# Performance work log

Hardware: AMD Instinct MI355X
Metric: run time of the kernel (lower is better)

Reference implementation:

```python
import jax, jax.numpy as jnp
import numpy as np

N = 65536      # collocation points
HID = 256      # hidden_dim
D = 3          # input_dim (x, y, t)
O = 2          # output_dim (streamfunction s, pressure p)


def _xavier(k, shape):
    fan_out, fan_in = shape
    std = (2.0 / (fan_in + fan_out)) ** 0.5
    return std * jax.random.normal(k, shape, dtype=jnp.float32)


def setup_inputs() -> dict:
    key = jax.random.key(0)
    ks = jax.random.split(key, 16)
    z = lambda n: jnp.zeros((n,), dtype=jnp.float32)
    return {
        "x": jax.random.normal(ks[0], (N,), dtype=jnp.float32),
        "y": jax.random.normal(ks[1], (N,), dtype=jnp.float32),
        "t": jax.random.normal(ks[2], (N,), dtype=jnp.float32),
        "p": jax.random.normal(ks[3], (N,), dtype=jnp.float32),
        "u": jax.random.normal(ks[4], (N,), dtype=jnp.float32),
        "v": jax.random.normal(ks[5], (N,), dtype=jnp.float32),
        # shared trunk: 3 Linear+Tanh layers
        "W1": _xavier(ks[6], (HID, D)),   "b1": z(HID),
        "W2": _xavier(ks[7], (HID, HID)), "b2": z(HID),
        "W3": _xavier(ks[8], (HID, HID)), "b3": z(HID),
        # pde head
        "Wp1": _xavier(ks[9], (HID, HID)),  "bp1": z(HID),
        "Wp2": _xavier(ks[10], (O, HID)),   "bp2": z(O),
        # data head
        "Wd1": _xavier(ks[11], (HID, HID)), "bd1": z(HID),
        "Wd2": _xavier(ks[12], (O, HID)),   "bd2": z(O),
        "lam1": jnp.float32(1.0),
        "lam2": jnp.float32(0.2),
    }


def reference(x, y, t, p, u, v,
              W1, b1, W2, b2, W3, b3,
              Wp1, bp1, Wp2, bp2,
              Wd1, bd1, Wd2, bd2,
              lam1, lam2):
    def trunk(q):  # q: [3]
        h = jnp.tanh(W1 @ q + b1)
        h = jnp.tanh(W2 @ h + b2)
        h = jnp.tanh(W3 @ h + b3)
        return h

    def pde_out(q):
        return Wp2 @ jnp.tanh(Wp1 @ trunk(q) + bp1) + bp2  # [2]

    def data_out(q):
        return Wd2 @ jnp.tanh(Wd1 @ trunk(q) + bd1) + bd2  # [2]

    s_pde = lambda q: pde_out(q)[0]
    p_pde = lambda q: pde_out(q)[1]
    s_data = lambda q: data_out(q)[0]

    grad_s = jax.grad(s_pde)                 # [3]  (s_x, s_y, s_t)
    hess_s = jax.jacfwd(grad_s)              # [3,3]
    third_s = jax.jacfwd(hess_s)             # [3,3,3]

    def per_sample(q):
        g1 = grad_s(q)
        H2 = hess_s(q)
        T3 = third_s(q)
        gp = jax.grad(p_pde)(q)
        do = data_out(q)
        gsd = jax.grad(s_data)(q)

        u_ = g1[1]            # u = ds/dy
        v_ = -g1[0]           # v = -ds/dx
        u_x, u_y, u_t = H2[1, 0], H2[1, 1], H2[1, 2]
        v_x, v_y, v_t = -H2[0, 0], -H2[0, 1], -H2[0, 2]
        u_xx, u_yy = T3[1, 0, 0], T3[1, 1, 1]
        v_xx, v_yy = -T3[0, 0, 0], -T3[0, 1, 1]
        p_x, p_y = gp[0], gp[1]

        f_ = lam1 * (u_t + u_ * u_x + v_ * u_y) + p_x - lam2 * (u_xx + u_yy)
        g_ = lam1 * (v_t + u_ * v_x + v_ * v_y) + p_y - lam2 * (v_xx + v_yy)

        p_pred = do[1]        # data head pressure
        u_pred = gsd[1]       # d s_data / dy
        v_pred = -gsd[0]      # -d s_data / dx
        return p_pred, u_pred, v_pred, f_, g_

    q = jnp.stack([x, y, t], axis=1)  # [N, 3]
    p_pred, u_pred, v_pred, f_, g_ = jax.vmap(per_sample)(q)
    return p_pred, u_pred, v_pred, f_, g_
```

## Files before the change

### kernel.cpp

```cpp
#include <hip/hip_runtime.h>


#define N_PTS 65536
#define HID   256
#define TS    6
#define MROWS (TS * 13)
#define MT    5

typedef _Float16 half_t;
typedef __attribute__((ext_vector_type(8))) _Float16 half8;
typedef __attribute__((ext_vector_type(4))) float floatx4;

#define J_HI   0
#define REDBUF 39936
#define LDS_BYTES (REDBUF + 288)

struct alignas(4) hpair { half_t a, b; };

__device__ __forceinline__ float fast_tanh(float x) {
    float e = __builtin_amdgcn_exp2f(x * 2.885390081777927f);
    return 1.f - 2.f * __builtin_amdgcn_rcpf(e + 1.f);
}

__device__ __forceinline__ void tanh_jet(const float* u, float* h) {
    const float f  = fast_tanh(u[0]);
    const float f1 = 1.f - f * f;
    const float f2 = -2.f * f * f1;
    const float f3 = -2.f * f1 * f1 + 4.f * f * f * f1;
    const float ux = u[1], uy = u[2], ut = u[3];
    const float uxx = u[4], uxy = u[5], uyy = u[6], uxt = u[7], uyt = u[8];
    h[0] = f;
    h[1] = f1 * ux;  h[2] = f1 * uy;  h[3] = f1 * ut;
    h[4] = f2 * ux * ux + f1 * uxx;
    h[5] = f2 * ux * uy + f1 * uxy;
    h[6] = f2 * uy * uy + f1 * uyy;
    h[7] = f2 * ux * ut + f1 * uxt;
    h[8] = f2 * uy * ut + f1 * uyt;
    h[9]  = f3 * ux * ux * ux + 3.f * f2 * ux * uxx + f1 * u[9];
    h[10] = f3 * ux * ux * uy + f2 * (uxx * uy + 2.f * uxy * ux) + f1 * u[10];
    h[11] = f3 * ux * uy * uy + f2 * (uyy * ux + 2.f * uxy * uy) + f1 * u[11];
    h[12] = f3 * uy * uy * uy + 3.f * f2 * uy * uyy + f1 * u[12];
}

__global__ void prep_w(const float* __restrict__ W2, const float* __restrict__ W3,
                       const float* __restrict__ Wp1, const float* __restrict__ Wd1,
                       half_t* __restrict__ ws) {
    int idx = blockIdx.x * 256 + threadIdx.x;
#pragma unroll
    for (int r = 0; r < 4; ++r) {
        int e = idx + r * 65536;
        int m = e >> 16, i = e & 65535;
        const float* src = (m == 0) ? W2 : (m == 1) ? W3 : (m == 2) ? Wp1 : Wd1;
        float w = src[i];
        half_t hi = (half_t)w;
        half_t lo = (half_t)(w - (float)hi);
        int n = i >> 8, k = i & 255;
        int addr = (((n >> 4) * 8 + (k >> 5)) * 64 + ((k >> 3) & 3) * 16 + (n & 15)) * 8
                   + (k & 7);
        ws[m * 131072 + addr] = hi;
        ws[m * 131072 + 65536 + addr] = lo;
    }
}

__device__ __forceinline__ void load_B(const half_t* bh, int vo, int kb,
                                       half8 (&Bh)[4]) {
#pragma unroll
    for (int nt = 0; nt < 4; ++nt) {
        int off = nt * 4096 + kb * 512 + vo;
        Bh[nt] = *(const half8*)(bh + off);
    }
}

__device__ __forceinline__ void mfma_phase(const char* __restrict__ smem,
                                           const int (&mx)[MT], const int (&mr)[MT],
                                           int kb, int q,
                                           const half8 (&Bh)[4],
                                           floatx4 (&acc)[MT][4]) {
    const int kq = (kb * 4 + q) << 4;
    __builtin_amdgcn_s_setprio(1);
#pragma unroll
    for (int mt = 0; mt < MT; ++mt) {
        const int a = mr[mt] + (kq ^ mx[mt]);
        half8 Ah = *(const half8*)(smem + J_HI + a);
#pragma unroll
        for (int nt = 0; nt < 4; ++nt) {
            acc[mt][nt] = __builtin_amdgcn_mfma_f32_16x16x32_f16(Ah, Bh[nt], acc[mt][nt], 0, 0, 0);
        }
    }
    __builtin_amdgcn_s_setprio(0);
}

__device__ __forceinline__ void epilogue_roll(char* __restrict__ smem,
                                              const float* __restrict__ bias,
                                              int wave, int lane,
                                              floatx4 (&acc)[MT][4]) {
    const int n = wave * 64 + lane;
    const float bn = bias[n];
    const int lanebase = ((n >> 3) << 4) | ((n & 7) << 1);
    float cprev[16], ccur[16];
    const int s_lo[MT] = {0, 1, 2, 3, 4};
    const int s_hi[MT] = {0, 1, 2, 3, 5};
#pragma unroll
    for (int mt = 0; mt < MT; ++mt) {
        float tv[4][4];
#pragma unroll
        for (int j = 0; j < 4; ++j)
#pragma unroll
            for (int r = 0; r < 4; ++r) tv[j][r] = acc[mt][j][r];
#pragma unroll
        for (int r = 0; r < 4; ++r) {
            asm("v_permlane16_swap_b32 %0, %1" : "+v"(tv[0][r]), "+v"(tv[1][r]));
            asm("v_permlane16_swap_b32 %0, %1" : "+v"(tv[2][r]), "+v"(tv[3][r]));
            asm("v_permlane32_swap_b32 %0, %1" : "+v"(tv[0][r]), "+v"(tv[2][r]));
            asm("v_permlane32_swap_b32 %0, %1" : "+v"(tv[1][r]), "+v"(tv[3][r]));
        }
#pragma unroll
        for (int j = 0; j < 4; ++j)
#pragma unroll
            for (int r = 0; r < 4; ++r) ccur[j * 4 + r] = tv[j][r];
#pragma unroll
        for (int s = s_lo[mt]; s <= s_hi[mt]; ++s) {
            float u[13], h[13];
#pragma unroll
            for (int c = 0; c < 13; ++c) {
                const int row = 13 * s + c;
                u[c] = ((row >> 4) == mt) ? ccur[row & 15] : cprev[row & 15];
            }
            u[0] += bn;
            tanh_jet(u, h);
#pragma unroll
            for (int c = 0; c < 13; ++c) {
                const int m = 13 * s + c;
                const int off = m * 512 + (lanebase ^ ((m & 15) << 4));
                *(half_t*)(smem + J_HI + off) = (half_t)h[c];
            }
        }
#pragma unroll
        for (int i = 0; i < 16; ++i) cprev[i] = ccur[i];
    }
}

__device__ __forceinline__ void layer(char* __restrict__ smem,
                                      const half_t* bh,
                                      const float* __restrict__ bias,
                                      int wave, int lane, int vo, int q, int nl,
                                      const half_t* nbh,
                                      half8 (&P0h)[4],
                                      floatx4 (&acc)[MT][4]) {
    int mx[MT], mr[MT];
#pragma unroll
    for (int mt = 0; mt < MT; ++mt) {
        int m = mt * 16 + nl;
        if (m > MROWS - 1) m = MROWS - 1;
        mx[mt] = (m & 15) << 4;
        mr[mt] = m * 512;
    }
    half8 B1h[4], B2h[4];
    load_B(bh, vo, 1, B1h);
#pragma unroll
    for (int mt = 0; mt < MT; ++mt)
#pragma unroll
        for (int nt = 0; nt < 4; ++nt) acc[mt][nt] = floatx4{0.f, 0.f, 0.f, 0.f};
    mfma_phase(smem, mx, mr, 0, q, P0h, acc);
    load_B(bh, vo, 2, B2h);
    mfma_phase(smem, mx, mr, 1, q, B1h, acc);
#pragma unroll 1
    for (int kb = 2; kb < 8; kb += 2) {
        load_B(bh, vo, kb + 1, B1h);
        mfma_phase(smem, mx, mr, kb, q, B2h, acc);
        if (kb + 2 < 8) load_B(bh, vo, kb + 2, B2h);
        mfma_phase(smem, mx, mr, kb + 1, q, B1h, acc);
    }
    load_B(nbh, vo, 0, P0h);
    __syncthreads();
    epilogue_roll(smem, bias, wave, lane, acc);
    __syncthreads();
}

__device__ __forceinline__ void head_phase(const char* __restrict__ smem,
                                           const int (&mh)[2], int kb, int q,
                                           const half8 (&Bh)[4],
                                           floatx4 (&hacc)[2][4]) {
    __builtin_amdgcn_s_setprio(1);
#pragma unroll
    for (int ht = 0; ht < 2; ++ht) {
        const int a = mh[ht] * 512 + ((((kb * 4 + q) << 4)) ^ ((mh[ht] & 15) << 4));
        half8 Ah = *(const half8*)(smem + J_HI + a);
#pragma unroll
        for (int nt = 0; nt < 4; ++nt) {
            hacc[ht][nt] = __builtin_amdgcn_mfma_f32_16x16x32_f16(Ah, Bh[nt], hacc[ht][nt], 0, 0, 0);
        }
    }
    __builtin_amdgcn_s_setprio(0);
}

__global__ __launch_bounds__(256, 3) void pinn_mfma(
    const float* __restrict__ gx, const float* __restrict__ gy, const float* __restrict__ gt,
    const float* __restrict__ W1, const float* __restrict__ b1,
    const float* __restrict__ b2, const float* __restrict__ b3,
    const float* __restrict__ bp1, const float* __restrict__ Wp2,
    const float* __restrict__ bd1, const float* __restrict__ Wd2,
    const float* __restrict__ bd2,
    const float* __restrict__ lam1p, const float* __restrict__ lam2p,
    const half_t* __restrict__ wsw, float* __restrict__ out) {
    extern __shared__ char smem[];
    const int t = threadIdx.x;
    const int wave = t >> 6, lane = t & 63;
    const int q = lane >> 4, nl = lane & 15;
    const int base = blockIdx.x * TS;
    const int wo = __builtin_amdgcn_readfirstlane(wave) * 16384;
    const int vo = lane * 8;

    const half_t* W2h = wsw + wo;
    const half_t* W3h = wsw + 131072 + wo;
    const half_t* Wph = wsw + 2 * 131072 + wo;
    const half_t* Wdh = wsw + 3 * 131072 + wo;

    half8 P0h[4];
    load_B(W2h, vo, 0, P0h);

#pragma unroll 1
    for (int ii = 0; ii < 3; ++ii) {
        int p = ii * 256 + t;
        int s = p >> 7, j = (p & 127) * 2;
        int gi = base + s; if (gi >= N_PTS) gi = N_PTS - 1;
        float qx = gx[gi], qy = gy[gi], qt = gt[gi];
        float hv[2][13];
#pragma unroll
        for (int d = 0; d < 2; ++d) {
            int jj = j + d;
            float w0 = W1[3 * jj], w1 = W1[3 * jj + 1], w2 = W1[3 * jj + 2];
            float f = fast_tanh(w0 * qx + w1 * qy + w2 * qt + b1[jj]);
            float f1 = 1.f - f * f;
            float f2c = -2.f * f * f1;
            float f3c = -2.f * f1 * f1 + 4.f * f * f * f1;
            float* h = hv[d];
            h[0] = f; h[1] = f1 * w0; h[2] = f1 * w1; h[3] = f1 * w2;
            h[4] = f2c * w0 * w0; h[5] = f2c * w0 * w1; h[6] = f2c * w1 * w1;
            h[7] = f2c * w0 * w2; h[8] = f2c * w1 * w2;
            h[9]  = f3c * w0 * w0 * w0; h[10] = f3c * w0 * w0 * w1;
            h[11] = f3c * w0 * w1 * w1; h[12] = f3c * w1 * w1 * w1;
        }
#pragma unroll
        for (int c = 0; c < 13; ++c) {
            int m = s * 13 + c;
            int off = m * 512 + ((((j) >> 3) ^ (m & 15)) << 4) + ((j & 7) << 1);
            half_t hA = (half_t)hv[0][c], hB = (half_t)hv[1][c];
            *(hpair*)(smem + J_HI + off) = hpair{hA, hB};
        }
    }
    __syncthreads();

    floatx4 acc[MT][4];

    layer(smem, W2h, b2, wave, lane, vo, q, nl, W3h, P0h, acc);
    layer(smem, W3h, b3, wave, lane, vo, q, nl, Wdh, P0h, acc);

    {
        int ch = (nl & 3) == 3 ? 0 : (nl & 3);
        int mh[2];
        mh[0] = (nl >> 2) * 13 + ch;
        {
            int s1 = 4 + (nl >> 2);
            mh[1] = (s1 < TS) ? s1 * 13 + ch : 52;
        }
        floatx4 hacc[2][4];
#pragma unroll
        for (int ht = 0; ht < 2; ++ht)
#pragma unroll
            for (int nt = 0; nt < 4; ++nt) hacc[ht][nt] = floatx4{0.f, 0.f, 0.f, 0.f};
        head_phase(smem, mh, 0, q, P0h, hacc);
#pragma unroll 1
        for (int kb = 1; kb < 8; ++kb) {
            half8 Bh[4];
            load_B(Wdh, vo, kb, Bh);
            head_phase(smem, mh, kb, q, Bh, hacc);
        }
        load_B(Wph, vo, 0, P0h);
        float* rb = (float*)(smem + REDBUF);
#pragma unroll
        for (int ht = 0; ht < 2; ++ht) {
            float pp = 0, up = 0, vp = 0;
#pragma unroll
            for (int nt = 0; nt < 4; ++nt) {
                int n = wave * 64 + nt * 16 + nl;
                floatx4 a = hacc[ht][nt];
                float f = fast_tanh(a.x + bd1[n]);
                float f1 = 1.f - f * f;
                float hdx = f1 * a.y, hdy = f1 * a.z;
                float w0 = Wd2[n], w1 = Wd2[HID + n];
                pp += w1 * f;
                up += w0 * hdy;
                vp -= w0 * hdx;
            }
#pragma unroll
            for (int msk = 1; msk < 16; msk <<= 1) {
                pp += __shfl_xor(pp, msk, 64);
                up += __shfl_xor(up, msk, 64);
                vp += __shfl_xor(vp, msk, 64);
            }
            int s = ht * 4 + q;
            if (nl == 0 && s < TS) {
                rb[(s * 4 + wave) * 3 + 0] = pp;
                rb[(s * 4 + wave) * 3 + 1] = up;
                rb[(s * 4 + wave) * 3 + 2] = vp;
            }
        }
        __syncthreads();
        if (t < TS && base + t < N_PTS) {
            float P = 0, U = 0, V = 0;
#pragma unroll
            for (int w = 0; w < 4; ++w) {
                P += rb[(t * 4 + w) * 3 + 0];
                U += rb[(t * 4 + w) * 3 + 1];
                V += rb[(t * 4 + w) * 3 + 2];
            }
            out[0 * N_PTS + base + t] = P + bd2[1];
            out[1 * N_PTS + base + t] = U;
            out[2 * N_PTS + base + t] = V;
        }
    }

    layer(smem, Wph, bp1, wave, lane, vo, q, nl, Wdh, P0h, acc);

    {
        int s = t >> 5, gl = t & 31;
        if (s < TS) {
            floatx4 w0a = *(const floatx4*)(Wp2 + gl * 8);
            floatx4 w0b = *(const floatx4*)(Wp2 + gl * 8 + 4);
            floatx4 w1a = *(const floatx4*)(Wp2 + HID + gl * 8);
            floatx4 w1b = *(const floatx4*)(Wp2 + HID + gl * 8 + 4);
            float wr0[8] = {w0a.x, w0a.y, w0a.z, w0a.w, w0b.x, w0b.y, w0b.z, w0b.w};
            float wr1[8] = {w1a.x, w1a.y, w1a.z, w1a.w, w1b.x, w1b.y, w1b.z, w1b.w};
            float S[13], px = 0.f, py = 0.f;
#pragma unroll
            for (int c = 0; c < 13; ++c) {
                const int m = s * 13 + c;
                const int off = m * 512 + ((gl ^ (m & 15)) << 4);
                half8 hv = *(const half8*)(smem + J_HI + off);
                float p = 0.f, p2 = 0.f;
#pragma unroll
                for (int e = 0; e < 8; ++e) {
                    float val = (float)hv[e];
                    p += val * wr0[e];
                    if (c == 1 || c == 2) p2 += val * wr1[e];
                }
#pragma unroll
                for (int msk = 1; msk < 32; msk <<= 1) p += __shfl_xor(p, msk, 64);
                S[c] = p;
                if (c == 1) {
#pragma unroll
                    for (int msk = 1; msk < 32; msk <<= 1) p2 += __shfl_xor(p2, msk, 64);
                    px = p2;
                } else if (c == 2) {
#pragma unroll
                    for (int msk = 1; msk < 32; msk <<= 1) p2 += __shfl_xor(p2, msk, 64);
                    py = p2;
                }
            }
            if (gl == 0 && base + s < N_PTS) {
                const float lam1 = lam1p[0], lam2 = lam2p[0];
                const float u_ = S[2], v_ = -S[1];
                const float u_x = S[5], u_y = S[6], u_t = S[8];
                const float v_x = -S[4], v_y = -S[5], v_t = -S[7];
                const float u_xx = S[10], u_yy = S[12];
                const float v_xx = -S[9], v_yy = -S[11];
                const float f_ = lam1 * (u_t + u_ * u_x + v_ * u_y) + px - lam2 * (u_xx + u_yy);
                const float g_ = lam1 * (v_t + u_ * v_x + v_ * v_y) + py - lam2 * (v_xx + v_yy);
                out[3 * N_PTS + base + s] = f_;
                out[4 * N_PTS + base + s] = g_;
            }
        }
    }
}

extern "C" void kernel_launch(void* const* d_in, const int* in_sizes, int n_in,
                              void* d_out, int out_size, void* d_ws, size_t ws_size,
                              hipStream_t stream) {
    const float* x   = (const float*)d_in[0];
    const float* y   = (const float*)d_in[1];
    const float* tt  = (const float*)d_in[2];
    const float* W1  = (const float*)d_in[6];
    const float* b1  = (const float*)d_in[7];
    const float* W2  = (const float*)d_in[8];
    const float* b2  = (const float*)d_in[9];
    const float* W3  = (const float*)d_in[10];
    const float* b3  = (const float*)d_in[11];
    const float* Wp1 = (const float*)d_in[12];
    const float* bp1 = (const float*)d_in[13];
    const float* Wp2 = (const float*)d_in[14];
    const float* Wd1 = (const float*)d_in[16];
    const float* bd1 = (const float*)d_in[17];
    const float* Wd2 = (const float*)d_in[18];
    const float* bd2 = (const float*)d_in[19];
    const float* l1  = (const float*)d_in[20];
    const float* l2  = (const float*)d_in[21];
    float* out = (float*)d_out;
    half_t* wsw = (half_t*)d_ws;

    prep_w<<<256, 256, 0, stream>>>(W2, W3, Wp1, Wd1, wsw);

    (void)hipFuncSetAttribute((const void*)pinn_mfma,
                              hipFuncAttributeMaxDynamicSharedMemorySize,
                              (int)LDS_BYTES);
    pinn_mfma<<<(N_PTS + TS - 1) / TS, 256, LDS_BYTES, stream>>>(
        x, y, tt, W1, b1, b2, b3, bp1, Wp2, bd1, Wd2, bd2, l1, l2, wsw, out);
}
```

Baseline: 571.4 us.

## Shrink per-block tile from 6 to 4 samples to remove padded MFMA rows

Each block now handles 4 collocation points instead of 6. That gives 52 jet rows across 4 MFMA M-tiles (64 rows) instead of 78 rows across 5 tiles (80 rows). The head pass needs only one M-tile, and the bounds checks are gone because 65536 divides evenly by 4. The aim is less wasted MFMA work per sample and less LDS per block. In exchange, the per-layer weight loads are shared by fewer samples, so weight traffic per point rises, and there are more blocks to launch.

```diff
diff --git a/kernel.cpp b/kernel.cpp
--- a/kernel.cpp
+++ b/kernel.cpp
@@ -3,17 +3,17 @@
 
 #define N_PTS 65536
 #define HID   256
-#define TS    6
+#define TS    4
 #define MROWS (TS * 13)
-#define MT    5
+#define MT    4
 
 typedef _Float16 half_t;
 typedef __attribute__((ext_vector_type(8))) _Float16 half8;
 typedef __attribute__((ext_vector_type(4))) float floatx4;
 
 #define J_HI   0
-#define REDBUF 39936
-#define LDS_BYTES (REDBUF + 288)
+#define REDBUF 26624
+#define LDS_BYTES (REDBUF + 192)
 
 struct alignas(4) hpair { half_t a, b; };
 
@@ -98,8 +98,6 @@
     const float bn = bias[n];
     const int lanebase = ((n >> 3) << 4) | ((n & 7) << 1);
     float cprev[16], ccur[16];
-    const int s_lo[MT] = {0, 1, 2, 3, 4};
-    const int s_hi[MT] = {0, 1, 2, 3, 5};
 #pragma unroll
     for (int mt = 0; mt < MT; ++mt) {
         float tv[4][4];
@@ -118,22 +116,19 @@
         for (int j = 0; j < 4; ++j)
 #pragma unroll
             for (int r = 0; r < 4; ++r) ccur[j * 4 + r] = tv[j][r];
-#pragma unroll
-        for (int s = s_lo[mt]; s <= s_hi[mt]; ++s) {
-            float u[13], h[13];
-#pragma unroll
-            for (int c = 0; c < 13; ++c) {
-                const int row = 13 * s + c;
-                u[c] = ((row >> 4) == mt) ? ccur[row & 15] : cprev[row & 15];
-            }
-            u[0] += bn;
-            tanh_jet(u, h);
-#pragma unroll
-            for (int c = 0; c < 13; ++c) {
-                const int m = 13 * s + c;
-                const int off = m * 512 + (lanebase ^ ((m & 15) << 4));
-                *(half_t*)(smem + J_HI + off) = (half_t)h[c];
-            }
+        float u[13], h[13];
+#pragma unroll
+        for (int c = 0; c < 13; ++c) {
+            const int row = 13 * mt + c;
+            u[c] = ((row >> 4) == mt) ? ccur[row & 15] : cprev[row & 15];
+        }
+        u[0] += bn;
+        tanh_jet(u, h);
+#pragma unroll
+        for (int c = 0; c < 13; ++c) {
+            const int m = 13 * mt + c;
+            const int off = m * 512 + (lanebase ^ ((m & 15) << 4));
+            *(half_t*)(smem + J_HI + off) = (half_t)h[c];
         }
 #pragma unroll
         for (int i = 0; i < 16; ++i) cprev[i] = ccur[i];
@@ -178,18 +173,15 @@
 }
 
 __device__ __forceinline__ void head_phase(const char* __restrict__ smem,
-                                           const int (&mh)[2], int kb, int q,
+                                           int mrh, int mxh, int kb, int q,
                                            const half8 (&Bh)[4],
-                                           floatx4 (&hacc)[2][4]) {
+                                           floatx4 (&hacc)[4]) {
     __builtin_amdgcn_s_setprio(1);
-#pragma unroll
-    for (int ht = 0; ht < 2; ++ht) {
-        const int a = mh[ht] * 512 + ((((kb * 4 + q) << 4)) ^ ((mh[ht] & 15) << 4));
-        half8 Ah = *(const half8*)(smem + J_HI + a);
-#pragma unroll
-        for (int nt = 0; nt < 4; ++nt) {
-            hacc[ht][nt] = __builtin_amdgcn_mfma_f32_16x16x32_f16(Ah, Bh[nt], hacc[ht][nt], 0, 0, 0);
-        }
+    const int a = mrh + (((kb * 4 + q) << 4) ^ mxh);
+    half8 Ah = *(const half8*)(smem + J_HI + a);
+#pragma unroll
+    for (int nt = 0; nt < 4; ++nt) {
+        hacc[nt] = __builtin_amdgcn_mfma_f32_16x16x32_f16(Ah, Bh[nt], hacc[nt], 0, 0, 0);
     }
     __builtin_amdgcn_s_setprio(0);
 }
@@ -220,11 +212,10 @@
     load_B(W2h, vo, 0, P0h);
 
 #pragma unroll 1
-    for (int ii = 0; ii < 3; ++ii) {
+    for (int ii = 0; ii < 2; ++ii) {
         int p = ii * 256 + t;
         int s = p >> 7, j = (p & 127) * 2;
-        int gi = base + s; if (gi >= N_PTS) gi = N_PTS - 1;
-        float qx = gx[gi], qy = gy[gi], qt = gt[gi];
+        float qx = gx[base + s], qy = gy[base + s], qt = gt[base + s];
         float hv[2][13];
 #pragma unroll
         for (int d = 0; d < 2; ++d) {
@@ -258,33 +249,26 @@
 
     {
         int ch = (nl & 3) == 3 ? 0 : (nl & 3);
-        int mh[2];
-        mh[0] = (nl >> 2) * 13 + ch;
-        {
-            int s1 = 4 + (nl >> 2);
-            mh[1] = (s1 < TS) ? s1 * 13 + ch : 52;
-        }
-        floatx4 hacc[2][4];
-#pragma unroll
-        for (int ht = 0; ht < 2; ++ht)
-#pragma unroll
-            for (int nt = 0; nt < 4; ++nt) hacc[ht][nt] = floatx4{0.f, 0.f, 0.f, 0.f};
-        head_phase(smem, mh, 0, q, P0h, hacc);
+        int mh = (nl >> 2) * 13 + ch;
+        const int mxh = (mh & 15) << 4, mrh = mh * 512;
+        floatx4 hacc[4];
+#pragma unroll
+        for (int nt = 0; nt < 4; ++nt) hacc[nt] = floatx4{0.f, 0.f, 0.f, 0.f};
+        head_phase(smem, mrh, mxh, 0, q, P0h, hacc);
 #pragma unroll 1
         for (int kb = 1; kb < 8; ++kb) {
             half8 Bh[4];
             load_B(Wdh, vo, kb, Bh);
-            head_phase(smem, mh, kb, q, Bh, hacc);
+            head_phase(smem, mrh, mxh, kb, q, Bh, hacc);
         }
         load_B(Wph, vo, 0, P0h);
         float* rb = (float*)(smem + REDBUF);
-#pragma unroll
-        for (int ht = 0; ht < 2; ++ht) {
+        {
             float pp = 0, up = 0, vp = 0;
 #pragma unroll
             for (int nt = 0; nt < 4; ++nt) {
                 int n = wave * 64 + nt * 16 + nl;
-                floatx4 a = hacc[ht][nt];
+                floatx4 a = hacc[nt];
                 float f = fast_tanh(a.x + bd1[n]);
                 float f1 = 1.f - f * f;
                 float hdx = f1 * a.y, hdy = f1 * a.z;
@@ -299,15 +283,14 @@
                 up += __shfl_xor(up, msk, 64);
                 vp += __shfl_xor(vp, msk, 64);
             }
-            int s = ht * 4 + q;
-            if (nl == 0 && s < TS) {
-                rb[(s * 4 + wave) * 3 + 0] = pp;
-                rb[(s * 4 + wave) * 3 + 1] = up;
-                rb[(s * 4 + wave) * 3 + 2] = vp;
+            if (nl == 0) {
+                rb[(q * 4 + wave) * 3 + 0] = pp;
+                rb[(q * 4 + wave) * 3 + 1] = up;
+                rb[(q * 4 + wave) * 3 + 2] = vp;
             }
         }
         __syncthreads();
-        if (t < TS && base + t < N_PTS) {
+        if (t < TS) {
             float P = 0, U = 0, V = 0;
 #pragma unroll
             for (int w = 0; w < 4; ++w) {
@@ -358,7 +341,7 @@
                     py = p2;
                 }
             }
-            if (gl == 0 && base + s < N_PTS) {
+            if (gl == 0) {
                 const float lam1 = lam1p[0], lam2 = lam2p[0];
                 const float u_ = S[2], v_ = -S[1];
                 const float u_x = S[5], u_y = S[6], u_t = S[8];
@@ -403,6 +386,6 @@
     (void)hipFuncSetAttribute((const void*)pinn_mfma,
                               hipFuncAttributeMaxDynamicSharedMemorySize,
                               (int)LDS_BYTES);
-    pinn_mfma<<<(N_PTS + TS - 1) / TS, 256, LDS_BYTES, stream>>>(
+    pinn_mfma<<<N_PTS / TS, 256, LDS_BYTES, stream>>>(
         x, y, tt, W1, b1, b2, b3, bp1, Wp2, bd1, Wd2, bd2, l1, l2, wsw, out);
 }
```

Result: slower. 603.9 us (+5.7%).
